# Performance work log

Hardware: AMD Instinct MI355X
Metric: run time of the kernel (lower is better)

## Reference

```python
import jax, jax.numpy as jnp
import numpy as np

NEG_SLOPE = 0.01  # torch F.leaky_relu default

def _leaky(v):
    return jnp.where(v > 0, v, NEG_SLOPE * v)

def _gcn_conv(h, W, b, row, col, n_nodes):
    # PyG GCNConv with add_self_loops=True, symmetric normalization:
    # out = D^{-1/2} (A + I) D^{-1/2} (h @ W) + b,  deg includes self loop (+1)
    xw = h @ W                                            # [N, H]
    deg = jnp.zeros((n_nodes,), xw.dtype).at[col].add(1.0) + 1.0
    dis = jax.lax.rsqrt(deg)
    norm = dis[row] * dis[col]                            # [E]
    agg = jnp.zeros_like(xw).at[col].add(norm[:, None] * xw[row])
    agg = agg + xw * (1.0 / deg)[:, None]                 # self-loop term: dis_i^2 = 1/deg_i
    return agg + b

def setup_inputs() -> dict:
    key = jax.random.key(0)
    ks = jax.random.split(key, 16)
    N, E, EL = 100000, 1600000, 200000
    IN, H, EA = 256, 64, 8
    s = 0.05
    return {
        "x": jax.random.normal(ks[0], (N, IN), jnp.float32),
        "edge_index": jax.random.randint(ks[1], (2, E), 0, N, jnp.int64),
        "edge_label_index": jax.random.randint(ks[2], (2, EL), 0, N, jnp.int64),
        "edge_attr": jax.random.normal(ks[3], (EL, EA), jnp.float32),
        "W1": jax.random.normal(ks[4], (IN, 128), jnp.float32) * s,
        "b1": jnp.zeros((128,), jnp.float32),
        "W2": jax.random.normal(ks[5], (128, H), jnp.float32) * s,
        "b2": jnp.zeros((H,), jnp.float32),
        "Wg1": jax.random.normal(ks[6], (H, H), jnp.float32) * s,
        "bg1": jnp.zeros((H,), jnp.float32),
        "Wg2": jax.random.normal(ks[7], (H, H), jnp.float32) * s,
        "bg2": jnp.zeros((H,), jnp.float32),
        "Wp": jax.random.normal(ks[8], (2 * H + EA, 1), jnp.float32) * s,
        "bp": jnp.zeros((1,), jnp.float32),
    }

def reference(x, edge_index, edge_label_index, edge_attr,
              W1, b1, W2, b2, Wg1, bg1, Wg2, bg2, Wp, bp):
    n_nodes = x.shape[0]
    row, col = edge_index[0], edge_index[1]
    # preprocess MLP (dropout p=0.0 -> identity)
    h = _leaky(x @ W1 + b1)
    h = _leaky(h @ W2 + b2)
    # two GCN layers
    h = _leaky(_gcn_conv(h, Wg1, bg1, row, col, n_nodes))
    h = _leaky(_gcn_conv(h, Wg2, bg2, row, col, n_nodes))
    # edge scoring head: gather-concat-linear
    h_src = h[edge_label_index[0]]
    h_dst = h[edge_label_index[1]]
    combined = jnp.concatenate([h_src, h_dst, edge_attr], axis=1)
    out = (combined @ Wp + bp).reshape(-1)
    return (out, h)
```

## Files before the change

kernel.cpp:

```cpp
#include <hip/hip_runtime.h>
#include <hip/hip_bf16.h>

typedef __attribute__((ext_vector_type(8))) short bf16x8;
typedef __attribute__((ext_vector_type(4))) float f32x4;

#define BSHIFT 8
#define BW 256
#define NSTR 8
#define BCAP 768
#define LCAP 24
#define KEDGE 16

__device__ __forceinline__ float lk(float v) { return v > 0.f ? v : 0.01f * v; }

__device__ __forceinline__ short f2b(float v) {
  union { __hip_bfloat16 h; short s; } u;
  u.h = __float2bfloat16(v);
  return u.s;
}
__device__ __forceinline__ float loadF(const void* p, size_t i, int f32) {
  return f32 ? ((const float*)p)[i]
             : __bfloat162float(((const __hip_bfloat16*)p)[i]);
}
__device__ __forceinline__ void storeF(void* p, size_t i, int f32, float v) {
  if (f32) ((float*)p)[i] = v;
  else     ((__hip_bfloat16*)p)[i] = __float2bfloat16(v);
}
__device__ __forceinline__ float blo(unsigned u) {
  union { unsigned u; float f; } c; c.u = u << 16; return c.f;
}
__device__ __forceinline__ float bhi(unsigned u) {
  union { unsigned u; float f; } c; c.u = u & 0xffff0000u; return c.f;
}

__global__ void detect_kernel(const unsigned short* __restrict__ x,
                              const int* __restrict__ ei, int* __restrict__ flags) {
  int t = threadIdx.x;
  unsigned short u = x[t];
  int ex = (u >> 7) & 0xFF;
  if (ex >= 0xC0) atomicOr(&flags[0], 1);
  if (t < 128 && ei[2 * t + 1] != 0) atomicOr(&flags[1], 1);
}

__global__ __launch_bounds__(64) void pack_all(const void* __restrict__ W1,
                                               const void* __restrict__ W2,
                                               const void* __restrict__ G1,
                                               const void* __restrict__ G2,
                                               __hip_bfloat16* __restrict__ P1,
                                               __hip_bfloat16* __restrict__ P2,
                                               __hip_bfloat16* __restrict__ PG1,
                                               __hip_bfloat16* __restrict__ PG2,
                                               const int* __restrict__ flags) {
  int f32 = flags[0] != 0;
  int b = blockIdx.x;
  const void* W; __hip_bfloat16* P; int KS, N, ks, ct;
  if (b < 64)      { W = W1; P = P1;  KS = 8; N = 128; int c = b;      ks = c & 7; ct = c >> 3; }
  else if (b < 80) { W = W2; P = P2;  KS = 4; N = 64;  int c = b - 64; ks = c & 3; ct = c >> 2; }
  else if (b < 88) { W = G1; P = PG1; KS = 2; N = 64;  int c = b - 80; ks = c & 1; ct = c >> 1; }
  else             { W = G2; P = PG2; KS = 2; N = 64;  int c = b - 88; ks = c & 1; ct = c >> 1; }
  int lane = threadIdx.x;
  int g = lane >> 4, m = lane & 15;
  size_t base = ((size_t)(ct * KS + ks) * 64 + (size_t)lane) * 8;
#pragma unroll
  for (int j = 0; j < 8; ++j)
    P[base + j] = __float2bfloat16(
        loadF(W, (size_t)(ks * 32 + g * 8 + j) * N + (size_t)(ct * 16 + m), f32));
}

__global__ __launch_bounds__(256) void gemm_fused12(const void* __restrict__ A,
                                                    const __hip_bfloat16* __restrict__ Bp1,
                                                    const void* __restrict__ b1,
                                                    const __hip_bfloat16* __restrict__ Bp2,
                                                    const void* __restrict__ b2,
                                                    __hip_bfloat16* __restrict__ Out,
                                                    int M, const int* __restrict__ flags) {
  constexpr int K1 = 256, CPR1 = K1 / 8;
  __shared__ char xtile[32 * K1 * 2];
  __shared__ char h1t[32 * 128 * 2];
  int f32 = flags[0] != 0;
  int tid = threadIdx.x;
  int lane = tid & 63;
  int w = tid >> 6;
  int m = lane & 15, g = lane >> 4;
  int row0 = blockIdx.x << 5;

  if (f32) {
    constexpr int PP = K1 / 64;
    float4 sr[2 * PP];
#pragma unroll
    for (int j = 0; j < PP; ++j) {
      int q = j * 256 + tid;
      int r = q / CPR1, pc = q - r * CPR1;
      int gr = row0 + r; if (gr >= M) gr = M - 1;
      const float* src = (const float*)A + (size_t)gr * K1 + (size_t)pc * 8;
      sr[2 * j]     = *(const float4*)src;
      sr[2 * j + 1] = *(const float4*)(src + 4);
    }
#pragma unroll
    for (int j = 0; j < PP; ++j) {
      int q = j * 256 + tid;
      int r = q / CPR1, pc = q - r * CPR1;
      bf16x8 ov;
      ov[0] = f2b(sr[2 * j].x);     ov[1] = f2b(sr[2 * j].y);
      ov[2] = f2b(sr[2 * j].z);     ov[3] = f2b(sr[2 * j].w);
      ov[4] = f2b(sr[2 * j + 1].x); ov[5] = f2b(sr[2 * j + 1].y);
      ov[6] = f2b(sr[2 * j + 1].z); ov[7] = f2b(sr[2 * j + 1].w);
      *(bf16x8*)(xtile + (size_t)r * (K1 * 2) + (size_t)((pc ^ (r & 7)) * 16)) = ov;
    }
  } else {
    constexpr int PERW = 32 * CPR1 / 4;
#pragma unroll
    for (int i = 0; i < PERW; i += 64) {
      int p = w * PERW + i + lane;
      int r = p / CPR1, pc = p - r * CPR1;
      int gr = row0 + r; if (gr >= M) gr = M - 1;
      const char* src = (const char*)A + (size_t)gr * (K1 * 2) +
                        (size_t)((pc ^ (r & 7)) * 16);
      char* dst = xtile + (size_t)(w * PERW + i) * 16;
      __builtin_amdgcn_global_load_lds(
          (const __attribute__((address_space(1))) void*)src,
          (__attribute__((address_space(3))) void*)dst, 16, 0, 0);
    }
  }
  __syncthreads();

  {
    const __hip_bfloat16* bbase = Bp1 + ((size_t)(w * 2) * 8 * 64 + (size_t)lane) * 8;
    f32x4 accs[2][2];
#pragma unroll
    for (int tt = 0; tt < 2; ++tt)
#pragma unroll
      for (int cc = 0; cc < 2; ++cc) accs[tt][cc] = (f32x4){0, 0, 0, 0};
#pragma unroll
    for (int ks = 0; ks < 8; ++ks) {
      bf16x8 a[2];
#pragma unroll
      for (int tt = 0; tt < 2; ++tt) {
        int r = tt * 16 + m;
        int c = ks * 4 + g;
        a[tt] = *(const bf16x8*)(xtile + (size_t)r * (K1 * 2) +
                                 (size_t)((c ^ (r & 7)) * 16));
      }
      const __hip_bfloat16* bb = bbase + (size_t)ks * 64 * 8;
#pragma unroll
      for (int cc = 0; cc < 2; ++cc) {
        bf16x8 b = *(const bf16x8*)(bb + (size_t)cc * 8 * 64 * 8);
#pragma unroll
        for (int tt = 0; tt < 2; ++tt)
          accs[tt][cc] = __builtin_amdgcn_mfma_f32_16x16x32_bf16(a[tt], b, accs[tt][cc], 0, 0, 0);
      }
    }
    float bv[2];
#pragma unroll
    for (int cc = 0; cc < 2; ++cc)
      bv[cc] = loadF(b1, (size_t)((w * 2 + cc) * 16 + m), f32);
#pragma unroll
    for (int tt = 0; tt < 2; ++tt) {
#pragma unroll
      for (int r = 0; r < 4; ++r) {
        int row = tt * 16 + g * 4 + r;
#pragma unroll
        for (int cc = 0; cc < 2; ++cc) {
          float v = lk(accs[tt][cc][r] + bv[cc]);
          int colb = ((w * 2 + cc) * 16 + m) * 2;
          int ch = colb >> 4, off = colb & 15;
          *(__hip_bfloat16*)(h1t + (size_t)row * 256 +
                             (size_t)((ch ^ (row & 7)) * 16) + off) =
              __float2bfloat16(v);
        }
      }
    }
  }
  __syncthreads();

  {
    const __hip_bfloat16* bbase = Bp2 + ((size_t)w * 4 * 64 + (size_t)lane) * 8;
    f32x4 accs[2];
    accs[0] = (f32x4){0, 0, 0, 0};
    accs[1] = (f32x4){0, 0, 0, 0};
#pragma unroll
    for (int ks = 0; ks < 4; ++ks) {
      bf16x8 a[2];
#pragma unroll
      for (int tt = 0; tt < 2; ++tt) {
        int r = tt * 16 + m;
        int c = ks * 4 + g;
        a[tt] = *(const bf16x8*)(h1t + (size_t)r * 256 +
                                 (size_t)((c ^ (r & 7)) * 16));
      }
      const __hip_bfloat16* bb = bbase + (size_t)ks * 64 * 8;
      bf16x8 b = *(const bf16x8*)bb;
#pragma unroll
      for (int tt = 0; tt < 2; ++tt)
        accs[tt] = __builtin_amdgcn_mfma_f32_16x16x32_bf16(a[tt], b, accs[tt], 0, 0, 0);
    }
    float bv = loadF(b2, (size_t)(w * 16 + m), f32);
#pragma unroll
    for (int tt = 0; tt < 2; ++tt) {
#pragma unroll
      for (int r = 0; r < 4; ++r) {
        int ro = row0 + tt * 16 + g * 4 + r;
        if (ro < M) {
          int col = w * 16 + m;
          Out[(size_t)ro * 64 + col] = __float2bfloat16(lk(accs[tt][r] + bv));
        }
      }
    }
  }
}

template <int KS, int CT>
__global__ __launch_bounds__(256) void gemm_bt(const void* __restrict__ A,
                                               const __hip_bfloat16* __restrict__ Bp,
                                               const void* __restrict__ bias,
                                               void* __restrict__ Out, int out_bf16,
                                               __hip_bfloat16* __restrict__ Yout,
                                               const float* __restrict__ dinv,
                                               int M, int N, int act,
                                               const int* __restrict__ flags) {
  constexpr int K = KS * 32;
  constexpr int CPR = K / 8;
  __shared__ char tile[32 * K * 2];
  int tid = threadIdx.x;
  int lane = tid & 63;
  int w = tid >> 6;
  int m = lane & 15, g = lane >> 4;
  int row0 = blockIdx.x << 5;

  {
    constexpr int PERW = 32 * CPR / 4;
#pragma unroll
    for (int i = 0; i < PERW; i += 64) {
      int p = w * PERW + i + lane;
      int r = p / CPR, pc = p - r * CPR;
      int gr = row0 + r; if (gr >= M) gr = M - 1;
      const char* src = (const char*)A + (size_t)gr * (K * 2) +
                        (size_t)((pc ^ (r & 7)) * 16);
      char* dst = tile + (size_t)(w * PERW + i) * 16;
      __builtin_amdgcn_global_load_lds(
          (const __attribute__((address_space(1))) void*)src,
          (__attribute__((address_space(3))) void*)dst, 16, 0, 0);
    }
  }
  __syncthreads();

  const __hip_bfloat16* bbase = Bp + ((size_t)(w * CT) * KS * 64 + (size_t)lane) * 8;
  f32x4 accs[2][CT];
#pragma unroll
  for (int tt = 0; tt < 2; ++tt)
#pragma unroll
    for (int cc = 0; cc < CT; ++cc) accs[tt][cc] = (f32x4){0, 0, 0, 0};

#pragma unroll
  for (int ks = 0; ks < KS; ++ks) {
    bf16x8 a[2];
#pragma unroll
    for (int tt = 0; tt < 2; ++tt) {
      int r = tt * 16 + m;
      int c = ks * 4 + g;
      a[tt] = *(const bf16x8*)(tile + (size_t)r * (K * 2) +
                               (size_t)((c ^ (r & 7)) * 16));
    }
    const __hip_bfloat16* bb = bbase + (size_t)ks * 64 * 8;
#pragma unroll
    for (int cc = 0; cc < CT; ++cc) {
      bf16x8 b = *(const bf16x8*)(bb + (size_t)cc * KS * 64 * 8);
#pragma unroll
      for (int tt = 0; tt < 2; ++tt)
        accs[tt][cc] = __builtin_amdgcn_mfma_f32_16x16x32_bf16(a[tt], b, accs[tt][cc], 0, 0, 0);
    }
  }

  int f32 = flags[0] != 0;
  float bv[CT];
#pragma unroll
  for (int cc = 0; cc < CT; ++cc)
    bv[cc] = bias ? loadF(bias, (size_t)((w * CT + cc) * 16 + m), f32) : 0.f;
#pragma unroll
  for (int tt = 0; tt < 2; ++tt) {
#pragma unroll
    for (int r = 0; r < 4; ++r) {
      int ro = row0 + tt * 16 + g * 4 + r;
      if (ro < M) {
        float di = Yout ? dinv[ro] : 0.f;
#pragma unroll
        for (int cc = 0; cc < CT; ++cc) {
          int col = (w * CT + cc) * 16 + m;
          float v = accs[tt][cc][r] + bv[cc];
          if (act) v = lk(v);
          if (Out) {
            if (out_bf16) ((__hip_bfloat16*)Out)[(size_t)ro * N + col] = __float2bfloat16(v);
            else          ((float*)Out)[(size_t)ro * N + col] = v;
          }
          if (Yout) Yout[(size_t)ro * N + col] = __float2bfloat16(v * di);
        }
      }
    }
  }
}

__global__ __launch_bounds__(256) void bin_kernel(const int* __restrict__ ei,
                                                  int* __restrict__ cur,
                                                  int2* __restrict__ rec,
                                                  int E, int NB,
                                                  const int* __restrict__ flags) {
  extern __shared__ int lds[];
  int* bcnt = lds;
  int* gbase = lds + NB;
  int2* bins = (int2*)(lds + 2 * NB);
  int i64 = flags[1] == 0;
  int stripe = __builtin_amdgcn_s_getreg(63508) & (NSTR - 1);
  int t = threadIdx.x;
  const int perRound = 256 * KEDGE;
  for (int base = blockIdx.x * perRound; base < E; base += gridDim.x * perRound) {
    for (int b = t; b < NB; b += 256) bcnt[b] = 0;
    __syncthreads();
#pragma unroll 1
    for (int k = 0; k < KEDGE; ++k) {
      int i = base + k * 256 + t;
      if (i < E) {
        int r, c;
        if (i64) {
          r = ((const int2*)ei)[i].x;
          c = ((const int2*)ei)[(size_t)E + i].x;
        } else {
          r = ei[i];
          c = ei[(size_t)E + i];
        }
        int b = c >> BSHIFT;
        int pos = atomicAdd(&bcnt[b], 1);
        if (pos < LCAP) {
          bins[b * LCAP + pos] = make_int2(r, c);
        } else {
          int bs = b * NSTR + stripe;
          int slot = atomicAdd(&cur[bs], 1);
          if (slot < BCAP) rec[(size_t)bs * BCAP + slot] = make_int2(r, c);
        }
      }
    }
    __syncthreads();
    for (int b = t; b < NB; b += 256) {
      int n = min(bcnt[b], LCAP);
      if (n > 0) gbase[b] = atomicAdd(&cur[b * NSTR + stripe], n);
    }
    __syncthreads();
    int lane = t & 63, w = t >> 6;
    for (int b = w; b < NB; b += 4) {
      int n = min(bcnt[b], LCAP);
      if (n == 0) continue;
      int gb = gbase[b];
      size_t sb = (size_t)(b * NSTR + stripe) * BCAP;
      if (lane < n && gb + lane < BCAP)
        rec[sb + gb + lane] = bins[b * LCAP + lane];
    }
    __syncthreads();
  }
}

__global__ __launch_bounds__(512) void place_kernel(const int2* __restrict__ rec,
                                                    const int* __restrict__ cur,
                                                    int* __restrict__ rowptr,
                                                    int* __restrict__ csr,
                                                    float* __restrict__ dinv, int Nn) {
  int b = blockIdx.x;
  int lo = b << BSHIFT;
  int t = threadIdx.x;
  __shared__ int cnt[BW];
  __shared__ int sc[BW];
  __shared__ int cursor[BW];
  __shared__ int red[512];
  int part = 0;
  for (int i = t; i < b * NSTR; i += 512) part += min(cur[i], BCAP);
  red[t] = part;
  if (t < BW) cnt[t] = 0;
  __syncthreads();
  for (int o = 256; o > 0; o >>= 1) {
    if (t < o) red[t] += red[t + o];
    __syncthreads();
  }
  int base = red[0];
#pragma unroll 1
  for (int s = 0; s < NSTR; ++s) {
    int n = min(cur[b * NSTR + s], BCAP);
    const int2* rp = rec + (size_t)(b * NSTR + s) * BCAP;
    for (int j = t; j < n; j += 512) atomicAdd(&cnt[rp[j].y - lo], 1);
  }
  __syncthreads();
  int v = 0;
  if (t < BW) { v = cnt[t]; sc[t] = v; }
  __syncthreads();
  for (int o = 1; o < BW; o <<= 1) {
    int a = (t >= o && t < BW) ? sc[t - o] : 0;
    __syncthreads();
    if (t < BW) sc[t] += a;
    __syncthreads();
  }
  if (t < BW) {
    int col = lo + t;
    if (col < Nn) {
      rowptr[col] = base + sc[t];
      dinv[col] = rsqrtf((float)v + 1.0f);
    }
    cursor[t] = base + sc[t] - v;
  }
  __syncthreads();
#pragma unroll 1
  for (int s = 0; s < NSTR; ++s) {
    int n = min(cur[b * NSTR + s], BCAP);
    const int2* rp = rec + (size_t)(b * NSTR + s) * BCAP;
    for (int j = t; j < n; j += 512) {
      int2 e = rp[j];
      int pos = atomicAdd(&cursor[e.y - lo], 1);
      csr[pos] = e.x;
    }
  }
}

__global__ __launch_bounds__(256) void gather_kernel(const __hip_bfloat16* __restrict__ y,
                                                     const int* __restrict__ csr,
                                                     const int* __restrict__ rowptr,
                                                     const float* __restrict__ dinv,
                                                     const void* __restrict__ bias,
                                                     void* __restrict__ outp, size_t obase,
                                                     int out_use_flag, int Nn,
                                                     float* __restrict__ ssrc,
                                                     float* __restrict__ sdst,
                                                     const void* __restrict__ Wp,
                                                     const int* __restrict__ flags) {
  int f32 = flags[0] != 0;
  int of32 = out_use_flag ? f32 : 0;
  int lane = threadIdx.x & 63;
  int w = (blockIdx.x * blockDim.x + threadIdx.x) >> 6;
  if (2 * w >= Nn) return;
  int half = lane >> 5;
  int hl = lane & 31;
  int hb = half << 5;
  int node = 2 * w + half;
  int alive = node < Nn;
  int nd = alive ? node : Nn - 1;
  int s = (nd == 0) ? 0 : rowptr[nd - 1];
  int e = rowptr[nd];
  if (!alive) e = s;
  const unsigned* yu = (const unsigned*)y;
  float p0a = 0, p1a = 0, p0b = 0, p1b = 0;
  float p0c = 0, p1c = 0, p0d = 0, p1d = 0;
  for (int base = s; base < e; base += 32) {
    int cnt = e - base; if (cnt > 32) cnt = 32;
    int rl = (base + hl < e) ? csr[base + hl] : 0;
    int j = 0;
    for (; j + 8 <= cnt; j += 8) {
      int r0 = __shfl(rl, hb + j + 0, 64);
      int r1 = __shfl(rl, hb + j + 1, 64);
      int r2 = __shfl(rl, hb + j + 2, 64);
      int r3 = __shfl(rl, hb + j + 3, 64);
      int r4 = __shfl(rl, hb + j + 4, 64);
      int r5 = __shfl(rl, hb + j + 5, 64);
      int r6 = __shfl(rl, hb + j + 6, 64);
      int r7 = __shfl(rl, hb + j + 7, 64);
      unsigned u0 = yu[(unsigned)r0 * 32u + hl];
      unsigned u1 = yu[(unsigned)r1 * 32u + hl];
      unsigned u2 = yu[(unsigned)r2 * 32u + hl];
      unsigned u3 = yu[(unsigned)r3 * 32u + hl];
      unsigned u4 = yu[(unsigned)r4 * 32u + hl];
      unsigned u5 = yu[(unsigned)r5 * 32u + hl];
      unsigned u6 = yu[(unsigned)r6 * 32u + hl];
      unsigned u7 = yu[(unsigned)r7 * 32u + hl];
      p0a += blo(u0); p1a += bhi(u0);
      p0b += blo(u1); p1b += bhi(u1);
      p0c += blo(u2); p1c += bhi(u2);
      p0d += blo(u3); p1d += bhi(u3);
      p0a += blo(u4); p1a += bhi(u4);
      p0b += blo(u5); p1b += bhi(u5);
      p0c += blo(u6); p1c += bhi(u6);
      p0d += blo(u7); p1d += bhi(u7);
    }
    for (; j + 4 <= cnt; j += 4) {
      int r0 = __shfl(rl, hb + j + 0, 64);
      int r1 = __shfl(rl, hb + j + 1, 64);
      int r2 = __shfl(rl, hb + j + 2, 64);
      int r3 = __shfl(rl, hb + j + 3, 64);
      unsigned u0 = yu[(unsigned)r0 * 32u + hl];
      unsigned u1 = yu[(unsigned)r1 * 32u + hl];
      unsigned u2 = yu[(unsigned)r2 * 32u + hl];
      unsigned u3 = yu[(unsigned)r3 * 32u + hl];
      p0a += blo(u0); p1a += bhi(u0);
      p0b += blo(u1); p1b += bhi(u1);
      p0c += blo(u2); p1c += bhi(u2);
      p0d += blo(u3); p1d += bhi(u3);
    }
    for (; j < cnt; ++j) {
      int r0 = __shfl(rl, hb + j, 64);
      unsigned u0 = yu[(unsigned)r0 * 32u + hl];
      p0a += blo(u0); p1a += bhi(u0);
    }
  }
  float acc0 = (p0a + p0b) + (p0c + p0d);
  float acc1 = (p1a + p1b) + (p1c + p1d);
  unsigned un = yu[(unsigned)nd * 32u + hl];
  acc0 += blo(un); acc1 += bhi(un);
  float di = dinv[nd];
  int f = hl * 2;
  float v0 = lk(di * acc0 + loadF(bias, (size_t)f, f32));
  float v1 = lk(di * acc1 + loadF(bias, (size_t)(f + 1), f32));
  if (alive) {
    if (of32) {
      *(float2*)((float*)outp + obase + (size_t)node * 64 + f) = make_float2(v0, v1);
    } else {
      union { unsigned u; unsigned short ss[2]; } pk;
      pk.ss[0] = (unsigned short)f2b(v0);
      pk.ss[1] = (unsigned short)f2b(v1);
      *(unsigned*)((__hip_bfloat16*)outp + obase + (size_t)node * 64 + f) = pk.u;
    }
  }
  if (ssrc) {
    float q1 = v0 * loadF(Wp, (size_t)f, f32) + v1 * loadF(Wp, (size_t)(f + 1), f32);
    float q2 = v0 * loadF(Wp, (size_t)(64 + f), f32) + v1 * loadF(Wp, (size_t)(65 + f), f32);
#pragma unroll
    for (int o = 16; o > 0; o >>= 1) {
      q1 += __shfl_down(q1, o, 64);
      q2 += __shfl_down(q2, o, 64);
    }
    if (hl == 0 && alive) { ssrc[node] = q1; sdst[node] = q2; }
  }
}

__global__ __launch_bounds__(256) void edge_head_kernel(void* __restrict__ dout,
                                                        const int* __restrict__ eli,
                                                        const void* __restrict__ ea,
                                                        const float* __restrict__ ssrc,
                                                        const float* __restrict__ sdst,
                                                        const void* __restrict__ Wp,
                                                        const void* __restrict__ bp,
                                                        int EL, const int* __restrict__ flags) {
  int f32 = flags[0] != 0;
  int i64 = flags[1] == 0;
  int tid = blockIdx.x * blockDim.x + threadIdx.x;
  if (tid >= EL) return;
  int s, d;
  if (i64) {
    s = ((const int2*)eli)[tid].x;
    d = ((const int2*)eli)[(size_t)EL + tid].x;
  } else {
    s = eli[tid];
    d = eli[(size_t)EL + tid];
  }
  float acc = ssrc[s] + sdst[d] + loadF(bp, 0, f32);
  if (f32) {
    const float* eap = (const float*)ea + (size_t)tid * 8;
    float4 u0 = *(const float4*)eap;
    float4 u1 = *(const float4*)(eap + 4);
    acc += u0.x * loadF(Wp, 128, 1) + u0.y * loadF(Wp, 129, 1) +
           u0.z * loadF(Wp, 130, 1) + u0.w * loadF(Wp, 131, 1) +
           u1.x * loadF(Wp, 132, 1) + u1.y * loadF(Wp, 133, 1) +
           u1.z * loadF(Wp, 134, 1) + u1.w * loadF(Wp, 135, 1);
  } else {
    bf16x8 u = *(const bf16x8*)((const __hip_bfloat16*)ea + (size_t)tid * 8);
#pragma unroll
    for (int j = 0; j < 8; ++j) {
      union { short s; __hip_bfloat16 h; } cv; cv.s = u[j];
      acc += __bfloat162float(cv.h) * loadF(Wp, (size_t)(128 + j), 0);
    }
  }
  storeF(dout, (size_t)tid, f32, acc);
}

extern "C" void kernel_launch(void* const* d_in, const int* in_sizes, int n_in,
                              void* d_out, int out_size, void* d_ws, size_t ws_size,
                              hipStream_t stream) {
  const void* x   = d_in[0];
  const int* ei   = (const int*)d_in[1];
  const int* eli  = (const int*)d_in[2];
  const void* ea  = d_in[3];
  const void* W1  = d_in[4];
  const void* b1  = d_in[5];
  const void* W2  = d_in[6];
  const void* b2  = d_in[7];
  const void* Wg1 = d_in[8];
  const void* bg1 = d_in[9];
  const void* Wg2 = d_in[10];
  const void* bg2 = d_in[11];
  const void* Wp  = d_in[12];
  const void* bp  = d_in[13];

  const int Nn = in_sizes[0] / 256;
  const int E  = in_sizes[1] / 2;
  const int EL = in_sizes[2] / 2;
  const int NB = (Nn + BW - 1) >> BSHIFT;

  char* ws = (char*)d_ws;
  size_t off = 0;
  auto take = [&](size_t bytes) -> char* {
    char* p = ws + off;
    off = (off + bytes + 255) & ~(size_t)255;
    return p;
  };
  int*   flags  = (int*)take(256);
  int*   cur    = (int*)take((size_t)NB * NSTR * 4);
  int*   rowptr = (int*)take((size_t)Nn * 4);
  float* dinv   = (float*)take((size_t)Nn * 4);
  float* ssrc   = (float*)take((size_t)Nn * 4);
  float* sdst   = (float*)take((size_t)Nn * 4);
  int*   csr    = (int*)take((size_t)E * 4);
  int2*  rec    = (int2*)take((size_t)NB * NSTR * BCAP * 8);
  __hip_bfloat16* pW1 = (__hip_bfloat16*)take(256 * 128 * 2);
  __hip_bfloat16* pW2 = (__hip_bfloat16*)take(128 * 64 * 2);
  __hip_bfloat16* pG1 = (__hip_bfloat16*)take(64 * 64 * 2);
  __hip_bfloat16* pG2 = (__hip_bfloat16*)take(64 * 64 * 2);
  char* regionA = take((size_t)Nn * 128 * 4);
  char* regionB = take((size_t)Nn * 64 * 4);
  __hip_bfloat16* y = (__hip_bfloat16*)(regionA + (size_t)Nn * 64 * 4);
  __hip_bfloat16* h2 = (__hip_bfloat16*)regionB;
  __hip_bfloat16* h3 = (__hip_bfloat16*)regionB;

  hipMemsetAsync(flags, 0, 256 + (((size_t)NB * NSTR * 4 + 255) & ~(size_t)255), stream);
  detect_kernel<<<1, 256, 0, stream>>>((const unsigned short*)x, ei, flags);

  pack_all<<<96, 64, 0, stream>>>(W1, W2, Wg1, Wg2, pW1, pW2, pG1, pG2, flags);

  const int ldsbytes = NB * (8 + LCAP * 8);
  const int nbin = (E + 256 * KEDGE - 1) / (256 * KEDGE);
  bin_kernel<<<nbin, 256, ldsbytes, stream>>>(ei, cur, rec, E, NB, flags);
  place_kernel<<<NB, 512, 0, stream>>>(rec, cur, rowptr, csr, dinv, Nn);

  const int tblocks = (Nn + 31) / 32;
  gemm_fused12<<<tblocks, 256, 0, stream>>>(x, pW1, b1, pW2, b2, h2, Nn, flags);

  const int gwaves = (Nn + 1) / 2;
  const int gblocks = (gwaves + 3) / 4;
  gemm_bt<2, 1><<<tblocks, 256, 0, stream>>>(h2, pG1, nullptr, nullptr, 0, y, dinv,
                                             Nn, 64, 0, flags);
  gather_kernel<<<gblocks, 256, 0, stream>>>(y, csr, rowptr, dinv, bg1,
                                             h3, 0, 0, Nn,
                                             nullptr, nullptr, nullptr, flags);

  gemm_bt<2, 1><<<tblocks, 256, 0, stream>>>(h3, pG2, nullptr, nullptr, 0, y, dinv,
                                             Nn, 64, 0, flags);
  gather_kernel<<<gblocks, 256, 0, stream>>>(y, csr, rowptr, dinv, bg2,
                                             d_out, (size_t)EL, 1, Nn,
                                             ssrc, sdst, Wp, flags);

  edge_head_kernel<<<(EL + 255) / 256, 256, 0, stream>>>(d_out, eli, ea, ssrc, sdst,
                                                         Wp, bp, EL, flags);
}
```

Measured before the change: 361.6 us.

## Fuse GCN weight GEMMs into preceding MLP and gather kernels

The first GCN linear transform (h2 @ Wg1 scaled by dinv) now runs inside the fused MLP kernel from an LDS tile, so h2 is never written to global memory. The first gather and the second GCN GEMM are merged into one kernel that aggregates 32 nodes into LDS and then multiplies by Wg2. This removes two launches and the global round trips of h2 and h3. In exchange, gather_gemm assigns 8 nodes per wave-half pair with a serial loop of 4, which may lower gather parallelism and load balance compared with the original layout.

```diff
diff --git a/kernel.cpp b/kernel.cpp
--- a/kernel.cpp
+++ b/kernel.cpp
@@ -67,16 +67,19 @@
         loadF(W, (size_t)(ks * 32 + g * 8 + j) * N + (size_t)(ct * 16 + m), f32));
 }
 
-__global__ __launch_bounds__(256) void gemm_fused12(const void* __restrict__ A,
-                                                    const __hip_bfloat16* __restrict__ Bp1,
-                                                    const void* __restrict__ b1,
-                                                    const __hip_bfloat16* __restrict__ Bp2,
-                                                    const void* __restrict__ b2,
-                                                    __hip_bfloat16* __restrict__ Out,
-                                                    int M, const int* __restrict__ flags) {
+__global__ __launch_bounds__(256) void gemm_fused123(const void* __restrict__ A,
+                                                     const __hip_bfloat16* __restrict__ Bp1,
+                                                     const void* __restrict__ b1,
+                                                     const __hip_bfloat16* __restrict__ Bp2,
+                                                     const void* __restrict__ b2,
+                                                     const __hip_bfloat16* __restrict__ BpG,
+                                                     const float* __restrict__ dinv,
+                                                     __hip_bfloat16* __restrict__ Yout,
+                                                     int M, const int* __restrict__ flags) {
   constexpr int K1 = 256, CPR1 = K1 / 8;
   __shared__ char xtile[32 * K1 * 2];
   __shared__ char h1t[32 * 128 * 2];
+  __shared__ char h2t[32 * 64 * 2];
   int f32 = flags[0] != 0;
   int tid = threadIdx.x;
   int lane = tid & 63;
@@ -199,100 +202,47 @@
     for (int tt = 0; tt < 2; ++tt) {
 #pragma unroll
       for (int r = 0; r < 4; ++r) {
+        int row = tt * 16 + g * 4 + r;
+        float v = lk(accs[tt][r] + bv);
+        int colb = (w * 16 + m) * 2;
+        int ch = colb >> 4, off = colb & 15;
+        *(__hip_bfloat16*)(h2t + (size_t)row * 128 +
+                           (size_t)((ch ^ (row & 7)) * 16) + off) =
+            __float2bfloat16(v);
+      }
+    }
+  }
+  __syncthreads();
+
+  {
+    const __hip_bfloat16* bbase = BpG + ((size_t)w * 2 * 64 + (size_t)lane) * 8;
+    f32x4 accs[2];
+    accs[0] = (f32x4){0, 0, 0, 0};
+    accs[1] = (f32x4){0, 0, 0, 0};
+#pragma unroll
+    for (int ks = 0; ks < 2; ++ks) {
+      bf16x8 a[2];
+#pragma unroll
+      for (int tt = 0; tt < 2; ++tt) {
+        int r = tt * 16 + m;
+        int c = ks * 4 + g;
+        a[tt] = *(const bf16x8*)(h2t + (size_t)r * 128 +
+                                 (size_t)((c ^ (r & 7)) * 16));
+      }
+      const __hip_bfloat16* bb = bbase + (size_t)ks * 64 * 8;
+      bf16x8 b = *(const bf16x8*)bb;
+#pragma unroll
+      for (int tt = 0; tt < 2; ++tt)
+        accs[tt] = __builtin_amdgcn_mfma_f32_16x16x32_bf16(a[tt], b, accs[tt], 0, 0, 0);
+    }
+#pragma unroll
+    for (int tt = 0; tt < 2; ++tt) {
+#pragma unroll
+      for (int r = 0; r < 4; ++r) {
         int ro = row0 + tt * 16 + g * 4 + r;
         if (ro < M) {
           int col = w * 16 + m;
-          Out[(size_t)ro * 64 + col] = __float2bfloat16(lk(accs[tt][r] + bv));
-        }
-      }
-    }
-  }
-}
-
-template <int KS, int CT>
-__global__ __launch_bounds__(256) void gemm_bt(const void* __restrict__ A,
-                                               const __hip_bfloat16* __restrict__ Bp,
-                                               const void* __restrict__ bias,
-                                               void* __restrict__ Out, int out_bf16,
-                                               __hip_bfloat16* __restrict__ Yout,
-                                               const float* __restrict__ dinv,
-                                               int M, int N, int act,
-                                               const int* __restrict__ flags) {
-  constexpr int K = KS * 32;
-  constexpr int CPR = K / 8;
-  __shared__ char tile[32 * K * 2];
-  int tid = threadIdx.x;
-  int lane = tid & 63;
-  int w = tid >> 6;
-  int m = lane & 15, g = lane >> 4;
-  int row0 = blockIdx.x << 5;
-
-  {
-    constexpr int PERW = 32 * CPR / 4;
-#pragma unroll
-    for (int i = 0; i < PERW; i += 64) {
-      int p = w * PERW + i + lane;
-      int r = p / CPR, pc = p - r * CPR;
-      int gr = row0 + r; if (gr >= M) gr = M - 1;
-      const char* src = (const char*)A + (size_t)gr * (K * 2) +
-                        (size_t)((pc ^ (r & 7)) * 16);
-      char* dst = tile + (size_t)(w * PERW + i) * 16;
-      __builtin_amdgcn_global_load_lds(
-          (const __attribute__((address_space(1))) void*)src,
-          (__attribute__((address_space(3))) void*)dst, 16, 0, 0);
-    }
-  }
-  __syncthreads();
-
-  const __hip_bfloat16* bbase = Bp + ((size_t)(w * CT) * KS * 64 + (size_t)lane) * 8;
-  f32x4 accs[2][CT];
-#pragma unroll
-  for (int tt = 0; tt < 2; ++tt)
-#pragma unroll
-    for (int cc = 0; cc < CT; ++cc) accs[tt][cc] = (f32x4){0, 0, 0, 0};
-
-#pragma unroll
-  for (int ks = 0; ks < KS; ++ks) {
-    bf16x8 a[2];
-#pragma unroll
-    for (int tt = 0; tt < 2; ++tt) {
-      int r = tt * 16 + m;
-      int c = ks * 4 + g;
-      a[tt] = *(const bf16x8*)(tile + (size_t)r * (K * 2) +
-                               (size_t)((c ^ (r & 7)) * 16));
-    }
-    const __hip_bfloat16* bb = bbase + (size_t)ks * 64 * 8;
-#pragma unroll
-    for (int cc = 0; cc < CT; ++cc) {
-      bf16x8 b = *(const bf16x8*)(bb + (size_t)cc * KS * 64 * 8);
-#pragma unroll
-      for (int tt = 0; tt < 2; ++tt)
-        accs[tt][cc] = __builtin_amdgcn_mfma_f32_16x16x32_bf16(a[tt], b, accs[tt][cc], 0, 0, 0);
-    }
-  }
-
-  int f32 = flags[0] != 0;
-  float bv[CT];
-#pragma unroll
-  for (int cc = 0; cc < CT; ++cc)
-    bv[cc] = bias ? loadF(bias, (size_t)((w * CT + cc) * 16 + m), f32) : 0.f;
-#pragma unroll
-  for (int tt = 0; tt < 2; ++tt) {
-#pragma unroll
-    for (int r = 0; r < 4; ++r) {
-      int ro = row0 + tt * 16 + g * 4 + r;
-      if (ro < M) {
-        float di = Yout ? dinv[ro] : 0.f;
-#pragma unroll
-        for (int cc = 0; cc < CT; ++cc) {
-          int col = (w * CT + cc) * 16 + m;
-          float v = accs[tt][cc][r] + bv[cc];
-          if (act) v = lk(v);
-          if (Out) {
-            if (out_bf16) ((__hip_bfloat16*)Out)[(size_t)ro * N + col] = __float2bfloat16(v);
-            else          ((float*)Out)[(size_t)ro * N + col] = v;
-          }
-          if (Yout) Yout[(size_t)ro * N + col] = __float2bfloat16(v * di);
+          Yout[(size_t)ro * 64 + col] = __float2bfloat16(accs[tt][r] * dinv[ro]);
         }
       }
     }
@@ -416,32 +366,10 @@
   }
 }
 
-__global__ __launch_bounds__(256) void gather_kernel(const __hip_bfloat16* __restrict__ y,
-                                                     const int* __restrict__ csr,
-                                                     const int* __restrict__ rowptr,
-                                                     const float* __restrict__ dinv,
-                                                     const void* __restrict__ bias,
-                                                     void* __restrict__ outp, size_t obase,
-                                                     int out_use_flag, int Nn,
-                                                     float* __restrict__ ssrc,
-                                                     float* __restrict__ sdst,
-                                                     const void* __restrict__ Wp,
-                                                     const int* __restrict__ flags) {
-  int f32 = flags[0] != 0;
-  int of32 = out_use_flag ? f32 : 0;
-  int lane = threadIdx.x & 63;
-  int w = (blockIdx.x * blockDim.x + threadIdx.x) >> 6;
-  if (2 * w >= Nn) return;
-  int half = lane >> 5;
-  int hl = lane & 31;
-  int hb = half << 5;
-  int node = 2 * w + half;
-  int alive = node < Nn;
-  int nd = alive ? node : Nn - 1;
-  int s = (nd == 0) ? 0 : rowptr[nd - 1];
-  int e = rowptr[nd];
-  if (!alive) e = s;
-  const unsigned* yu = (const unsigned*)y;
+__device__ __forceinline__ void gather_node(const unsigned* __restrict__ yu,
+                                            const int* __restrict__ csr,
+                                            int s, int e, int hl, int hb,
+                                            float& acc0, float& acc1) {
   float p0a = 0, p1a = 0, p0b = 0, p1b = 0;
   float p0c = 0, p1c = 0, p0d = 0, p1d = 0;
   for (int base = s; base < e; base += 32) {
@@ -494,8 +422,118 @@
       p0a += blo(u0); p1a += bhi(u0);
     }
   }
-  float acc0 = (p0a + p0b) + (p0c + p0d);
-  float acc1 = (p1a + p1b) + (p1c + p1d);
+  acc0 = (p0a + p0b) + (p0c + p0d);
+  acc1 = (p1a + p1b) + (p1c + p1d);
+}
+
+__global__ __launch_bounds__(256) void gather_gemm(const __hip_bfloat16* __restrict__ y,
+                                                   const int* __restrict__ csr,
+                                                   const int* __restrict__ rowptr,
+                                                   const float* __restrict__ dinv,
+                                                   const void* __restrict__ bias,
+                                                   const __hip_bfloat16* __restrict__ BpG,
+                                                   __hip_bfloat16* __restrict__ Y2,
+                                                   int Nn, const int* __restrict__ flags) {
+  __shared__ char h3t[32 * 64 * 2];
+  int f32 = flags[0] != 0;
+  int tid = threadIdx.x;
+  int lane = tid & 63;
+  int hl = lane & 31;
+  int hb = (lane >> 5) << 5;
+  int hw = tid >> 5;
+  int row0 = blockIdx.x << 5;
+  const unsigned* yu = (const unsigned*)y;
+  int f = hl * 2;
+  float bv0 = loadF(bias, (size_t)f, f32);
+  float bv1 = loadF(bias, (size_t)(f + 1), f32);
+
+#pragma unroll 1
+  for (int k = 0; k < 4; ++k) {
+    int node = row0 + hw + 8 * k;
+    int alive = node < Nn;
+    int nd = alive ? node : Nn - 1;
+    int s = (nd == 0) ? 0 : rowptr[nd - 1];
+    int e = rowptr[nd];
+    if (!alive) e = s;
+    float acc0, acc1;
+    gather_node(yu, csr, s, e, hl, hb, acc0, acc1);
+    unsigned un = yu[(unsigned)nd * 32u + hl];
+    acc0 += blo(un); acc1 += bhi(un);
+    float di = dinv[nd];
+    float v0 = lk(di * acc0 + bv0);
+    float v1 = lk(di * acc1 + bv1);
+    int row = hw + 8 * k;
+    union { unsigned u; unsigned short ss[2]; } pk;
+    pk.ss[0] = (unsigned short)f2b(v0);
+    pk.ss[1] = (unsigned short)f2b(v1);
+    int colb = f * 2;
+    int ch = colb >> 4, off = colb & 15;
+    *(unsigned*)(h3t + (size_t)row * 128 + (size_t)((ch ^ (row & 7)) * 16) + off) = pk.u;
+  }
+  __syncthreads();
+
+  int w = tid >> 6;
+  int m = lane & 15, g = lane >> 4;
+  const __hip_bfloat16* bbase = BpG + ((size_t)w * 2 * 64 + (size_t)lane) * 8;
+  f32x4 accs[2];
+  accs[0] = (f32x4){0, 0, 0, 0};
+  accs[1] = (f32x4){0, 0, 0, 0};
+#pragma unroll
+  for (int ks = 0; ks < 2; ++ks) {
+    bf16x8 a[2];
+#pragma unroll
+    for (int tt = 0; tt < 2; ++tt) {
+      int r = tt * 16 + m;
+      int c = ks * 4 + g;
+      a[tt] = *(const bf16x8*)(h3t + (size_t)r * 128 +
+                               (size_t)((c ^ (r & 7)) * 16));
+    }
+    const __hip_bfloat16* bb = bbase + (size_t)ks * 64 * 8;
+    bf16x8 b = *(const bf16x8*)bb;
+#pragma unroll
+    for (int tt = 0; tt < 2; ++tt)
+      accs[tt] = __builtin_amdgcn_mfma_f32_16x16x32_bf16(a[tt], b, accs[tt], 0, 0, 0);
+  }
+#pragma unroll
+  for (int tt = 0; tt < 2; ++tt) {
+#pragma unroll
+    for (int r = 0; r < 4; ++r) {
+      int ro = row0 + tt * 16 + g * 4 + r;
+      if (ro < Nn) {
+        int col = w * 16 + m;
+        Y2[(size_t)ro * 64 + col] = __float2bfloat16(accs[tt][r] * dinv[ro]);
+      }
+    }
+  }
+}
+
+__global__ __launch_bounds__(256) void gather_kernel(const __hip_bfloat16* __restrict__ y,
+                                                     const int* __restrict__ csr,
+                                                     const int* __restrict__ rowptr,
+                                                     const float* __restrict__ dinv,
+                                                     const void* __restrict__ bias,
+                                                     void* __restrict__ outp, size_t obase,
+                                                     int Nn,
+                                                     float* __restrict__ ssrc,
+                                                     float* __restrict__ sdst,
+                                                     const void* __restrict__ Wp,
+                                                     const int* __restrict__ flags) {
+  int f32 = flags[0] != 0;
+  int lane = threadIdx.x & 63;
+  int w = (blockIdx.x * blockDim.x + threadIdx.x) >> 6;
+  if (2 * w >= Nn) return;
+  int half = lane >> 5;
+  int hl = lane & 31;
+  int hb = half << 5;
+  int node = 2 * w + half;
+  int alive = node < Nn;
+  int nd = alive ? node : Nn - 1;
+  int s = (nd == 0) ? 0 : rowptr[nd - 1];
+  int e = rowptr[nd];
+  if (!alive) e = s;
+  const unsigned* yu = (const unsigned*)y;
+  float acc0, acc1;
+  gather_node(yu, csr, s, e, hl, hb, acc0, acc1);
   unsigned un = yu[(unsigned)nd * 32u + hl];
   acc0 += blo(un); acc1 += bhi(un);
   float di = dinv[nd];
@@ -503,7 +541,7 @@
   float v0 = lk(di * acc0 + loadF(bias, (size_t)f, f32));
   float v1 = lk(di * acc1 + loadF(bias, (size_t)(f + 1), f32));
   if (alive) {
-    if (of32) {
+    if (f32) {
       *(float2*)((float*)outp + obase + (size_t)node * 64 + f) = make_float2(v0, v1);
     } else {
       union { unsigned u; unsigned short ss[2]; } pk;
@@ -512,16 +550,14 @@
       *(unsigned*)((__hip_bfloat16*)outp + obase + (size_t)node * 64 + f) = pk.u;
     }
   }
-  if (ssrc) {
-    float q1 = v0 * loadF(Wp, (size_t)f, f32) + v1 * loadF(Wp, (size_t)(f + 1), f32);
-    float q2 = v0 * loadF(Wp, (size_t)(64 + f), f32) + v1 * loadF(Wp, (size_t)(65 + f), f32);
-#pragma unroll
-    for (int o = 16; o > 0; o >>= 1) {
-      q1 += __shfl_down(q1, o, 64);
-      q2 += __shfl_down(q2, o, 64);
-    }
-    if (hl == 0 && alive) { ssrc[node] = q1; sdst[node] = q2; }
-  }
+  float q1 = v0 * loadF(Wp, (size_t)f, f32) + v1 * loadF(Wp, (size_t)(f + 1), f32);
+  float q2 = v0 * loadF(Wp, (size_t)(64 + f), f32) + v1 * loadF(Wp, (size_t)(65 + f), f32);
+#pragma unroll
+  for (int o = 16; o > 0; o >>= 1) {
+    q1 += __shfl_down(q1, o, 64);
+    q2 += __shfl_down(q2, o, 64);
+  }
+  if (hl == 0 && alive) { ssrc[node] = q1; sdst[node] = q2; }
 }
 
 __global__ __launch_bounds__(256) void edge_head_kernel(void* __restrict__ dout,
@@ -606,11 +642,8 @@
   __hip_bfloat16* pW2 = (__hip_bfloat16*)take(128 * 64 * 2);
   __hip_bfloat16* pG1 = (__hip_bfloat16*)take(64 * 64 * 2);
   __hip_bfloat16* pG2 = (__hip_bfloat16*)take(64 * 64 * 2);
-  char* regionA = take((size_t)Nn * 128 * 4);
-  char* regionB = take((size_t)Nn * 64 * 4);
-  __hip_bfloat16* y = (__hip_bfloat16*)(regionA + (size_t)Nn * 64 * 4);
-  __hip_bfloat16* h2 = (__hip_bfloat16*)regionB;
-  __hip_bfloat16* h3 = (__hip_bfloat16*)regionB;
+  __hip_bfloat16* y  = (__hip_bfloat16*)take((size_t)Nn * 64 * 2);
+  __hip_bfloat16* y2 = (__hip_bfloat16*)take((size_t)Nn * 64 * 2);
 
   hipMemsetAsync(flags, 0, 256 + (((size_t)NB * NSTR * 4 + 255) & ~(size_t)255), stream);
   detect_kernel<<<1, 256, 0, stream>>>((const unsigned short*)x, ei, flags);
@@ -623,20 +656,16 @@
   place_kernel<<<NB, 512, 0, stream>>>(rec, cur, rowptr, csr, dinv, Nn);
 
   const int tblocks = (Nn + 31) / 32;
-  gemm_fused12<<<tblocks, 256, 0, stream>>>(x, pW1, b1, pW2, b2, h2, Nn, flags);
+  gemm_fused123<<<tblocks, 256, 0, stream>>>(x, pW1, b1, pW2, b2, pG1, dinv, y,
+                                             Nn, flags);
+
+  gather_gemm<<<tblocks, 256, 0, stream>>>(y, csr, rowptr, dinv, bg1, pG2, y2,
+                                           Nn, flags);
 
   const int gwaves = (Nn + 1) / 2;
   const int gblocks = (gwaves + 3) / 4;
-  gemm_bt<2, 1><<<tblocks, 256, 0, stream>>>(h2, pG1, nullptr, nullptr, 0, y, dinv,
-                                             Nn, 64, 0, flags);
-  gather_kernel<<<gblocks, 256, 0, stream>>>(y, csr, rowptr, dinv, bg1,
-                                             h3, 0, 0, Nn,
-                                             nullptr, nullptr, nullptr, flags);
-
-  gemm_bt<2, 1><<<tblocks, 256, 0, stream>>>(h3, pG2, nullptr, nullptr, 0, y, dinv,
-                                             Nn, 64, 0, flags);
-  gather_kernel<<<gblocks, 256, 0, stream>>>(y, csr, rowptr, dinv, bg2,
-                                             d_out, (size_t)EL, 1, Nn,
+  gather_kernel<<<gblocks, 256, 0, stream>>>(y2, csr, rowptr, dinv, bg2,
+                                             d_out, (size_t)EL, Nn,
                                              ssrc, sdst, Wp, flags);
 
   edge_head_kernel<<<(EL + 255) / 256, 256, 0, stream>>>(d_out, eli, ea, ssrc, sdst,
```

Result: faster. 342.0 us (-5.4%).
